# Performance work log

Hardware: AMD Instinct MI355X
Metric: run time of the kernel (lower is better)

Reference implementation:

```python
import jax, jax.numpy as jnp
import numpy as np

B, T, IN_DIM, D, C = 64, 128, 300, 64, 10
NUM_LAYERS = 2   # recurrent_cells = [QRNNCell(d)] * num_layers -> SHARED cell params
BETA = 0.8       # QActivation beta; scale_factor=2 -> matrix square of rho


def _ortho(k, n, m):
    a = jax.random.normal(k, (n, n), dtype=jnp.float32)
    q, _ = jnp.linalg.qr(a)
    return q[:, :m]


def setup_inputs() -> dict:
    key = jax.random.key(0)
    ks = jax.random.split(key, 8)
    return {
        "x": jax.random.normal(ks[0], (B, T, IN_DIM), jnp.float32),
        "amp_w": jax.random.normal(ks[1], (IN_DIM, D), jnp.float32) * (1.0 / np.sqrt(IN_DIM)),
        "amp_b": jnp.zeros((D,), jnp.float32),
        "phase_w": jax.random.normal(ks[2], (IN_DIM, D), jnp.float32) * (1.0 / np.sqrt(IN_DIM)),
        "phase_b": jnp.zeros((D,), jnp.float32),
        "unitary_x": _ortho(ks[3], D, D),   # real orthogonal (Stiefel) unitary
        "unitary_h": _ortho(ks[4], D, D),
        "cell_lambda": jnp.zeros((), jnp.float32),
        "dense_w": _ortho(ks[5], D, C),     # orthonormal columns: D -> C subspace map
        "dense_lambda": jnp.zeros((), jnp.float32),
        "meas_kernel": jax.random.normal(ks[6], (C, C, 2), jnp.float32),  # complex measurement vectors
    }


def _uconj(U, r, i):
    # real unitary conjugation U rho U^T applied to complex rho = r + 1j*i
    return (jnp.einsum('pq,bqr,sr->bps', U, r, U),
            jnp.einsum('pq,bqr,sr->bps', U, i, U))


def _qactivation(r, i):
    # scale_factor=2: rho^2 (sharpens eigen-spectrum), trace-normalized; beta-mix with rho
    r2 = r @ r - i @ i
    i2 = r @ i + i @ r
    tr = jnp.trace(r2, axis1=-2, axis2=-1)[..., None, None]
    return BETA * r2 / tr + (1.0 - BETA) * r, BETA * i2 / tr + (1.0 - BETA) * i


def _run_layer(xs_r, xs_i, Ux, Uh, lam):
    # xs_*: [T,B,D,D]; sequential QRNN scan over time
    b, d = xs_r.shape[1], xs_r.shape[-1]
    h0 = (jnp.broadcast_to(jnp.eye(d, dtype=xs_r.dtype) / d, (b, d, d)),
          jnp.zeros((b, d, d), xs_r.dtype))
    def step(h, x):
        xr, xi = x
        hr, hi = h
        uxr, uxi = _uconj(Ux, xr, xi)
        uhr, uhi = _uconj(Uh, hr, hi)
        nr = lam * uxr + (1.0 - lam) * uhr
        ni = lam * uxi + (1.0 - lam) * uhi
        nr, ni = _qactivation(nr, ni)
        return (nr, ni), (nr, ni)
    _, (out_r, out_i) = jax.lax.scan(step, h0, (xs_r, xs_i))
    return out_r, out_i


def reference(x, amp_w, amp_b, phase_w, phase_b, unitary_x, unitary_h,
              cell_lambda, dense_w, dense_lambda, meas_kernel):
    # amplitude (L2-normalized) and phase projections
    amp = x @ amp_w + amp_b
    amp = amp / jnp.linalg.norm(amp, axis=-1, keepdims=True)
    phase = x @ phase_w + phase_b
    sr = amp * jnp.cos(phase)                      # ComplexMultiply -> [B,T,D]
    si = amp * jnp.sin(phase)
    # QOuter: pure density matrices rho = |s><s| -> [T,B,D,D]
    rr = jnp.einsum('btd,bte->tbde', sr, sr) + jnp.einsum('btd,bte->tbde', si, si)
    ri = jnp.einsum('btd,bte->tbde', si, sr) - jnp.einsum('btd,bte->tbde', sr, si)
    lam = jax.nn.sigmoid(cell_lambda)
    for _ in range(NUM_LAYERS):                    # shared cell params (list * num_layers)
        rr, ri = _run_layer(rr, ri, unitary_x, unitary_h, lam)
    # QDropout: identity in eval mode
    # QDense: sigma = W^T rho W, Lambda-mixed with I/C, trace-normalized
    c = dense_w.shape[1]
    sg_r = jnp.einsum('dc,tbde,ef->tbcf', dense_w, rr, dense_w)
    sg_i = jnp.einsum('dc,tbde,ef->tbcf', dense_w, ri, dense_w)
    dlam = jax.nn.sigmoid(dense_lambda)
    sg_r = dlam * sg_r + (1.0 - dlam) * jnp.eye(c, dtype=sg_r.dtype) / c
    sg_i = dlam * sg_i
    tr = jnp.trace(sg_r, axis1=-2, axis2=-1)[..., None, None]
    sg_r = sg_r / tr
    sg_i = sg_i / tr
    # QMeasurement: p_k = Re(<v_k| rho |v_k>) with unit-norm complex v_k
    vr, vi = meas_kernel[..., 0], meas_kernel[..., 1]
    nrm = jnp.sqrt(jnp.sum(vr * vr + vi * vi, axis=-1, keepdims=True))
    vr, vi = vr / nrm, vi / nrm
    p = (jnp.einsum('kc,kd,tbcd->tbk', vr, vr, sg_r)
         + jnp.einsum('kc,kd,tbcd->tbk', vi, vi, sg_r)
         - jnp.einsum('kc,kd,tbcd->tbk', vr, vi, sg_i)
         + jnp.einsum('kc,kd,tbcd->tbk', vi, vr, sg_i))
    return jnp.log(jnp.transpose(p, (1, 0, 2)))    # [B,T,C] log-probs
```

## Files before the change

kernel.cpp:

```cpp
#include <hip/hip_runtime.h>
#include <math.h>

#define B_ 64
#define T_ 128
#define INDIM 300
#define D_ 64
#define C_ 10
#define BETA_ 0.8f

typedef unsigned int u32;
typedef _Float16 half8 __attribute__((ext_vector_type(8)));
typedef float f32x4 __attribute__((ext_vector_type(4)));
typedef u32 u32x4 __attribute__((ext_vector_type(4)));
typedef u32 u32x2 __attribute__((ext_vector_type(2)));

#define GIDX(cb,kc,ln) ((((cb)*2+(kc))*64) + (ln))

struct Frag { half8 h, l; };

static __device__ __forceinline__ float sigmoidf_(float x){ return 1.f/(1.f+expf(-x)); }

static __device__ __forceinline__ float wave_sum(float v){
#pragma unroll
  for (int off = 32; off > 0; off >>= 1) v += __shfl_down(v, off);
  return v;
}

static __device__ __forceinline__ u32 pkh(_Float16 a, _Float16 b){
  unsigned short ba = __builtin_bit_cast(unsigned short, a);
  unsigned short bb = __builtin_bit_cast(unsigned short, b);
  return (u32)ba | ((u32)bb << 16);
}

static __device__ __forceinline__ void split4(const float* x, u32x2& hw, u32x2& lw){
  _Float16 h0=(_Float16)x[0], h1=(_Float16)x[1], h2=(_Float16)x[2], h3=(_Float16)x[3];
  _Float16 l0=(_Float16)(x[0]-(float)h0), l1=(_Float16)(x[1]-(float)h1);
  _Float16 l2=(_Float16)(x[2]-(float)h2), l3=(_Float16)(x[3]-(float)h3);
  hw[0]=pkh(h0,h1); hw[1]=pkh(h2,h3); lw[0]=pkh(l0,l1); lw[1]=pkh(l2,l3);
}

static __device__ __forceinline__ void up2v(u32 hw, u32 lw, float& v0, float& v1){
  _Float16 h0=__builtin_bit_cast(_Float16,(unsigned short)(hw & 0xffffu));
  _Float16 h1=__builtin_bit_cast(_Float16,(unsigned short)(hw >> 16));
  _Float16 l0=__builtin_bit_cast(_Float16,(unsigned short)(lw & 0xffffu));
  _Float16 l1=__builtin_bit_cast(_Float16,(unsigned short)(lw >> 16));
  v0 = (float)h0 + (float)l0;
  v1 = (float)h1 + (float)l1;
}

static __device__ __forceinline__ void mfma4(const Frag& a, const Frag& b, f32x4& acc){
  acc = __builtin_amdgcn_mfma_f32_16x16x32_f16(a.h, b.h, acc, 0, 0, 0);
  acc = __builtin_amdgcn_mfma_f32_16x16x32_f16(a.h, b.l, acc, 0, 0, 0);
  acc = __builtin_amdgcn_mfma_f32_16x16x32_f16(a.l, b.h, acc, 0, 0, 0);
}

static __device__ __forceinline__ Frag ldfrag(const u32* buf, int g, bool neg){
  u32x4 a = *reinterpret_cast<const u32x4*>(buf + g*4);
  u32x4 b = *reinterpret_cast<const u32x4*>(buf + 2048 + g*4);
  if (neg){
#pragma unroll
    for (int i=0;i<4;++i){ a[i]^=0x80008000u; b[i]^=0x80008000u; }
  }
  Frag f; f.h = __builtin_bit_cast(half8, a); f.l = __builtin_bit_cast(half8, b);
  return f;
}

static __device__ __forceinline__ Frag ldbg(const u32* FL, int grp, int lane){
  const u32* p = FL + ((size_t)(grp*64 + lane))*8;
  u32x4 a = *reinterpret_cast<const u32x4*>(p);
  u32x4 b = *reinterpret_cast<const u32x4*>(p+4);
  Frag f; f.h = __builtin_bit_cast(half8, a); f.l = __builtin_bit_cast(half8, b);
  return f;
}

static __device__ __forceinline__ void store_tile(u32* O, int ti, int tj, int h, int c15,
                                                  const float* x){
  const int s = h & 1;
  const int lp = c15 + 16*((2*ti + (h>>1)) & 3);
  const int g = GIDX(tj, ti>>1, lp);
  u32x2 hw, lw; split4(x, hw, lw);
  *reinterpret_cast<u32x2*>(O + g*4 + 2*s) = hw;
  *reinterpret_cast<u32x2*>(O + 2048 + g*4 + 2*s) = lw;
}

static __device__ __forceinline__ void read_tile(const u32* O, int ti, int tj, int h, int c15,
                                                 float* n){
  const int s = h & 1;
  const int lp = c15 + 16*((2*ti + (h>>1)) & 3);
  const int g = GIDX(tj, ti>>1, lp);
  u32x2 nh = *reinterpret_cast<const u32x2*>(O + g*4 + 2*s);
  u32x2 nl = *reinterpret_cast<const u32x2*>(O + 2048 + g*4 + 2*s);
  up2v(nh[0],nl[0],n[0],n[1]); up2v(nh[1],nl[1],n[2],n[3]);
}

__global__ __launch_bounds__(64) void proj_kernel(
    const float* __restrict__ x, const float* __restrict__ amp_w,
    const float* __restrict__ amp_b, const float* __restrict__ phase_w,
    const float* __restrict__ phase_b, const float* __restrict__ Ux,
    float* __restrict__ u_out) {
    __shared__ float xr[INDIM];
    __shared__ float s_r[D_], s_i[D_];
    const int bt = blockIdx.x;
    const int b = bt / T_, t = bt % T_;
    const float* xrow = x + (size_t)bt * INDIM;
    for (int i = threadIdx.x; i < INDIM; i += 64) xr[i] = xrow[i];
    __syncthreads();
    const int d = threadIdx.x;
    float a = amp_b[d], p = phase_b[d];
    for (int k = 0; k < INDIM; ++k) {
        float xv = xr[k];
        a = fmaf(xv, amp_w[k * D_ + d], a);
        p = fmaf(xv, phase_w[k * D_ + d], p);
    }
    float sq = a * a;
    #pragma unroll
    for (int off = 32; off > 0; off >>= 1) sq += __shfl_xor(sq, off);
    float an = a / sqrtf(sq);
    s_r[d] = an * cosf(p);
    s_i[d] = an * sinf(p);
    __syncthreads();
    float ur = 0.f, ui = 0.f;
    const float* Uxrow = Ux + d * D_;
    for (int e = 0; e < D_; ++e) {
        float uv = Uxrow[e];
        ur = fmaf(uv, s_r[e], ur);
        ui = fmaf(uv, s_i[e], ui);
    }
    float* ub = u_out + ((size_t)t * B_ + b) * 128;
    ub[d] = ur;
    ub[64 + d] = ui;
}

__global__ __launch_bounds__(256) void setup_kernel(
    const float* __restrict__ Uh, const float* __restrict__ Ux,
    const float* __restrict__ W, const float* __restrict__ meas,
    u32* __restrict__ UhFL, u32* __restrict__ UxFL,
    u32* __restrict__ AB2FL, float* __restrict__ AB2p, float* __restrict__ ABt)
{
  const int tid = threadIdx.x;
  for (int wi = tid; wi < 4096; wi += 256){
    int off = wi & 7, g = wi >> 3;
    int lane_ = g & 63, cbkc = g >> 6;
    int cb = cbkc >> 1, kc = cbkc & 1;
    int wq = off & 3; bool isHi = off < 4;
    int k0 = 32*kc + 8*(lane_>>4) + 2*wq;
    int c  = 16*cb + (lane_&15);
    {
      float x0 = Uh[c*64 + k0], x1 = Uh[c*64 + k0 + 1];
      _Float16 h0=(_Float16)x0, h1=(_Float16)x1;
      UhFL[wi] = isHi ? pkh(h0,h1)
                      : pkh((_Float16)(x0-(float)h0), (_Float16)(x1-(float)h1));
    }
    {
      float x0 = Ux[c*64 + k0], x1 = Ux[c*64 + k0 + 1];
      _Float16 h0=(_Float16)x0, h1=(_Float16)x1;
      UxFL[wi] = isHi ? pkh(h0,h1)
                      : pkh((_Float16)(x0-(float)h0), (_Float16)(x1-(float)h1));
    }
  }
  __shared__ float invn[C_];
  if (tid < C_) {
    float s = 0.f;
    for (int j = 0; j < C_; ++j) {
      float vr = meas[(tid * C_ + j) * 2], vi = meas[(tid * C_ + j) * 2 + 1];
      s += vr * vr + vi * vi;
    }
    invn[tid] = 1.0f / sqrtf(s);
  }
  __syncthreads();
  for (int i = tid; i < D_ * 32; i += 256) {
    int dd = i >> 5, c = i & 31;
    float v = 0.f;
    if (c < C_) {
      float acc = 0.f;
      for (int j = 0; j < C_; ++j) acc = fmaf(W[dd * C_ + j], meas[(c * C_ + j) * 2], acc);
      v = acc * invn[c];
    } else if (c < 2 * C_) {
      int k = c - C_;
      float acc = 0.f;
      for (int j = 0; j < C_; ++j) acc = fmaf(W[dd * C_ + j], meas[(k * C_ + j) * 2 + 1], acc);
      v = acc * invn[k];
    } else if (c < 3 * C_) {
      v = W[dd * C_ + (c - 2 * C_)];
    }
    AB2p[i] = v;
  }
  __syncthreads();
  for (int wi = tid; wi < 2048; wi += 256){
    int off = wi & 7, g = wi >> 3;
    int lane_ = g & 63, cbkc = g >> 6;
    int cb = cbkc >> 1, kc = cbkc & 1;
    int wq = off & 3; bool isHi = off < 4;
    int k0 = 32*kc + 8*(lane_>>4) + 2*wq;
    int c  = 16*cb + (lane_&15);
    float x0 = AB2p[k0*32 + c], x1 = AB2p[(k0+1)*32 + c];
    _Float16 h0=(_Float16)x0, h1=(_Float16)x1;
    AB2FL[wi] = isHi ? pkh(h0,h1)
                     : pkh((_Float16)(x0-(float)h0), (_Float16)(x1-(float)h1));
  }
  for (int i = tid; i < 30*64; i += 256){
    int c = i >> 6, d = i & 63;
    ABt[i] = AB2p[d*32 + c];
  }
}

__global__ __launch_bounds__(512) void qrnn_kernel(
    const float* __restrict__ u_in,
    const u32* __restrict__ UhFL, const u32* __restrict__ UxFL,
    const u32* __restrict__ AB2FL, const float* __restrict__ ABt,
    const float* __restrict__ cell_lambda, const float* __restrict__ dense_lambda,
    float* __restrict__ out)
{
  __shared__ __align__(16) u32 ds[9*4096];
  __shared__ float u_lds[128];
  __shared__ float scrN1[8], scrNp[8], scrQ[12];

  const int tid = threadIdx.x;
  const int lane = tid & 63;
  const int w = tid >> 6;
  const int h = lane >> 4;
  const int c15 = lane & 15;
  const int bidx = blockIdx.x;
  const float lam = sigmoidf_(cell_lambda[0]);
  const float clm = 1.f - lam;
  const float dlam = sigmoidf_(dense_lambda[0]);

  u32* const B0 = ds + 0*4096;
  u32* const B1 = ds + 1*4096;
  u32* const B2 = ds + 2*4096;
  u32* const B3 = ds + 3*4096;
  u32* const B4 = ds + 4*4096;
  u32* const B5 = ds + 5*4096;
  u32* const B6 = ds + 6*4096;
  u32* const B7 = ds + 7*4096;
  u32* const B8 = ds + 8*4096;
  float* const Zt = reinterpret_cast<float*>(B6);

  const u32 one64 = (u32)__builtin_bit_cast(unsigned short, (_Float16)0.015625f);
  for (int wi = tid; wi < 4096; wi += 512){
    u32 vR = 0u;
    if (wi < 2048){
      int g = wi >> 2, wq = wi & 3;
      int lane_ = g & 63, cbkc = g >> 6;
      int cb = cbkc >> 1, kc = cbkc & 1;
      int k0 = 32*kc + 8*(lane_>>4) + 2*wq;
      int c = 16*cb + (lane_&15);
      if (k0 == c)   vR |= one64;
      if (k0+1 == c) vR |= (one64 << 16);
    }
    B0[wi] = vR; B2[wi] = vR; B1[wi] = 0u; B3[wi] = 0u;
  }
  __syncthreads();

  for (int t = 0; t <= T_; ++t){
    const bool doMain = (t < T_);
    const bool doTail = (t > 0);
    const int par = t & 1;
    u32* const pH2I = par ? B4 : B3;
    u32* const pTXR = par ? B3 : B4;

    if (doMain){
      if (tid < 128) u_lds[tid] = u_in[((size_t)t*B_ + bidx)*128 + tid];
      const int comp = w>>2, ti = w&3;
      const u32* A = comp ? B1 : B0;
      Frag a0 = ldfrag(A, GIDX(ti,0,lane), false);
      Frag a1 = ldfrag(A, GIDX(ti,1,lane), false);
      u32* O = comp ? B5 : pTXR;
#pragma unroll
      for (int tj=0;tj<4;++tj){
        Frag b0 = ldbg(UhFL, tj*2+0, lane);
        Frag b1 = ldbg(UhFL, tj*2+1, lane);
        f32x4 acc = {0.f,0.f,0.f,0.f};
        mfma4(a0,b0,acc); mfma4(a1,b1,acc);
        float xv[4] = {acc[0],acc[1],acc[2],acc[3]};
        store_tile(O, ti, tj, h, c15, xv);
      }
    }
    if (doTail){
      const int rb = w;
      const int cb = rb&3;
      const u32* A = (rb<4) ? B2 : pH2I;
      Frag a0 = ldfrag(A, GIDX(cb,0,lane), false);
      Frag a1 = ldfrag(A, GIDX(cb,1,lane), false);
#pragma unroll
      for (int cz=0;cz<2;++cz){
        Frag b0 = ldbg(AB2FL, cz*2+0, lane);
        Frag b1 = ldbg(AB2FL, cz*2+1, lane);
        f32x4 za = {0.f,0.f,0.f,0.f};
        mfma4(a0,b0,za); mfma4(a1,b1,za);
        const int c = 16*cz + c15;
        if (c < 30){
          float* zp = Zt + c*129 + 16*rb + 4*h;
#pragma unroll
          for (int rr=0;rr<4;++rr) zp[rr] = za[rr];
        }
      }
    }
    __syncthreads();

    if (doMain){
      const int comp = w>>2, ti = w&3;
      const u32* A = comp ? B5 : pTXR;
      Frag a0 = ldfrag(A, GIDX(ti,0,lane), false);
      Frag a1 = ldfrag(A, GIDX(ti,1,lane), false);
      u32* O = comp ? B8 : B7;
      float uR[4], uI[4];
#pragma unroll
      for (int rr=0;rr<4;++rr){
        uR[rr] = u_lds[16*ti + 4*h + rr];
        uI[rr] = u_lds[64 + 16*ti + 4*h + rr];
      }
      float ss = 0.f;
#pragma unroll
      for (int tj=0;tj<4;++tj){
        Frag b0 = ldbg(UhFL, tj*2+0, lane);
        Frag b1 = ldbg(UhFL, tj*2+1, lane);
        f32x4 acc = {0.f,0.f,0.f,0.f};
        mfma4(a0,b0,acc); mfma4(a1,b1,acc);
        const float urc = u_lds[16*tj + c15], uic = u_lds[64 + 16*tj + c15];
        float xv[4];
#pragma unroll
        for (int rr=0;rr<4;++rr){
          float ov = comp ? (uI[rr]*urc - uR[rr]*uic) : (uR[rr]*urc + uI[rr]*uic);
          xv[rr] = lam*ov + clm*acc[rr];
          ss = fmaf(xv[rr], xv[rr], ss);
        }
        store_tile(O, ti, tj, h, c15, xv);
      }
      ss = wave_sum(ss);
      if (lane == 0) scrN1[w] = ss;
    }
    if (doTail){
      {
        const int k = w;
        float av = ABt[k*64 + lane], bv = ABt[(10+k)*64 + lane];
        float v = av*Zt[k*129 + lane] + bv*Zt[(10+k)*129 + lane]
                + av*Zt[(10+k)*129 + 64 + lane] - bv*Zt[k*129 + 64 + lane];
        v = wave_sum(v);
        if (lane == 0) scrQ[k] = v;
      }
      if (w < 2){
        const int k = 8 + w;
        float av = ABt[k*64 + lane], bv = ABt[(10+k)*64 + lane];
        float v = av*Zt[k*129 + lane] + bv*Zt[(10+k)*129 + lane]
                + av*Zt[(10+k)*129 + 64 + lane] - bv*Zt[k*129 + 64 + lane];
        v = wave_sum(v);
        if (lane == 0) scrQ[k] = v;
      } else if (w == 2){
        float v = 0.f;
#pragma unroll
        for (int cc=0; cc<10; ++cc)
          v = fmaf(ABt[(20+cc)*64 + lane], Zt[(20+cc)*129 + lane], v);
        v = wave_sum(v);
        if (lane == 0) scrQ[10] = v;
      }
    }
    __syncthreads();

    if (doMain){
      const int o = w>>2, tj = w&3;
      f32x4 acc[4];
#pragma unroll
      for (int i=0;i<4;++i) acc[i] = f32x4{0.f,0.f,0.f,0.f};
#pragma unroll
      for (int m=0;m<2;++m){
        const u32* Ab = m ? B8 : B7;
        const u32* Bb = o ? (m ? B7 : B8) : (m ? B8 : B7);
        const bool neg = (o==1) && (m==1);
#pragma unroll
        for (int kc=0;kc<2;++kc){
          Frag bf = ldfrag(Bb, GIDX(tj,kc,lane), false);
#pragma unroll
          for (int i=0;i<4;++i){
            Frag af = ldfrag(Ab, GIDX(i,kc,lane), neg);
            mfma4(af, bf, acc[i]);
          }
        }
      }
      const f32x4* sv = reinterpret_cast<const f32x4*>(scrN1);
      f32x4 s4 = sv[0] + sv[1];
      const float trv = s4[0]+s4[1]+s4[2]+s4[3];
      const float sb = BETA_/trv, cbm = 1.f - BETA_;
      const u32* Nsrc = o ? B8 : B7;
      u32* Od = o ? B1 : B0;
#pragma unroll
      for (int i=0;i<4;++i){
        float n[4]; read_tile(Nsrc, i, tj, h, c15, n);
        float xv[4];
#pragma unroll
        for (int rr=0;rr<4;++rr) xv[rr] = fmaf(sb, acc[i][rr], cbm*n[rr]);
        store_tile(Od, i, tj, h, c15, xv);
      }
    }
    if (doTail && tid < 10){
      float pnum = dlam*scrQ[tid] + (1.f-dlam)*0.1f;
      float pden = dlam*scrQ[10] + (1.f-dlam);
      out[((size_t)bidx*T_ + (t-1))*C_ + tid] = logf(pnum/pden);
    }
    __syncthreads();

    if (doMain){
      {
        const int g2 = w>>2, comp=(w>>1)&1, th=w&1;
        const u32* A = g2 ? (comp? pH2I : B2) : (comp? B1 : B0);
        const u32* FL = g2 ? UhFL : UxFL;
        u32* O = g2 ? (comp? B7 : B6) : (comp? B5 : pTXR);
        Frag a00 = ldfrag(A, GIDX(th,0,lane),   false);
        Frag a01 = ldfrag(A, GIDX(th,1,lane),   false);
        Frag a10 = ldfrag(A, GIDX(th+2,0,lane), false);
        Frag a11 = ldfrag(A, GIDX(th+2,1,lane), false);
#pragma unroll
        for (int tj=0;tj<4;++tj){
          Frag b0 = ldbg(FL, tj*2+0, lane);
          Frag b1 = ldbg(FL, tj*2+1, lane);
          f32x4 acc0 = {0.f,0.f,0.f,0.f};
          mfma4(a00,b0,acc0); mfma4(a01,b1,acc0);
          float xv0[4] = {acc0[0],acc0[1],acc0[2],acc0[3]};
          store_tile(O, th, tj, h, c15, xv0);
          f32x4 acc1 = {0.f,0.f,0.f,0.f};
          mfma4(a10,b0,acc1); mfma4(a11,b1,acc1);
          float xv1[4] = {acc1[0],acc1[1],acc1[2],acc1[3]};
          store_tile(O, th+2, tj, h, c15, xv1);
        }
      }
      __syncthreads();

      {
        const int comp = w>>2, ti = w&3;
        u32* O = comp ? pH2I : B8;
        const u32* AX = comp ? B5 : pTXR;
        const u32* AH = comp ? B7 : B6;
        Frag ax0 = ldfrag(AX, GIDX(ti,0,lane), false);
        Frag ax1 = ldfrag(AX, GIDX(ti,1,lane), false);
        Frag ah0 = ldfrag(AH, GIDX(ti,0,lane), false);
        Frag ah1 = ldfrag(AH, GIDX(ti,1,lane), false);
        float ss = 0.f;
#pragma unroll
        for (int tj=0;tj<4;++tj){
          f32x4 aX = {0.f,0.f,0.f,0.f};
          {
            Frag bx0 = ldbg(UxFL, tj*2+0, lane);
            Frag bx1 = ldbg(UxFL, tj*2+1, lane);
            mfma4(ax0,bx0,aX); mfma4(ax1,bx1,aX);
          }
          f32x4 aH = {0.f,0.f,0.f,0.f};
          {
            Frag bh0 = ldbg(UhFL, tj*2+0, lane);
            Frag bh1 = ldbg(UhFL, tj*2+1, lane);
            mfma4(ah0,bh0,aH); mfma4(ah1,bh1,aH);
          }
          float xv[4];
#pragma unroll
          for (int rr=0;rr<4;++rr){
            xv[rr] = lam*aX[rr] + clm*aH[rr];
            ss = fmaf(xv[rr], xv[rr], ss);
          }
          store_tile(O, ti, tj, h, c15, xv);
        }
        ss = wave_sum(ss);
        if (lane == 0) scrNp[w] = ss;
      }
      __syncthreads();

      {
        const int o = w>>2, tj = w&3;
        const u32* NPR = B8;
        const u32* NPI = pH2I;
        f32x4 acc[4];
#pragma unroll
        for (int i=0;i<4;++i) acc[i] = f32x4{0.f,0.f,0.f,0.f};
#pragma unroll
        for (int m=0;m<2;++m){
          const u32* Ab = m ? NPI : NPR;
          const u32* Bb = o ? (m ? NPR : NPI) : (m ? NPI : NPR);
          const bool neg = (o==1) && (m==1);
#pragma unroll
          for (int kc=0;kc<2;++kc){
            Frag bf = ldfrag(Bb, GIDX(tj,kc,lane), false);
#pragma unroll
            for (int i=0;i<4;++i){
              Frag af = ldfrag(Ab, GIDX(i,kc,lane), neg);
              mfma4(af, bf, acc[i]);
            }
          }
        }
        const f32x4* sv = reinterpret_cast<const f32x4*>(scrNp);
        f32x4 s4 = sv[0] + sv[1];
        const float trv = s4[0]+s4[1]+s4[2]+s4[3];
        const float sb = BETA_/trv, cbm = 1.f - BETA_;
        const u32* Nsrc = o ? NPI : NPR;
        u32* Od = o ? pTXR : B2;
#pragma unroll
        for (int i=0;i<4;++i){
          float n[4]; read_tile(Nsrc, i, tj, h, c15, n);
          float xv[4];
#pragma unroll
          for (int rr=0;rr<4;++rr) xv[rr] = fmaf(sb, acc[i][rr], cbm*n[rr]);
          store_tile(Od, i, tj, h, c15, xv);
        }
      }
      __syncthreads();
    }
  }
}

extern "C" void kernel_launch(void* const* d_in, const int* in_sizes, int n_in,
                              void* d_out, int out_size, void* d_ws, size_t ws_size,
                              hipStream_t stream) {
    const float* x       = (const float*)d_in[0];
    const float* amp_w   = (const float*)d_in[1];
    const float* amp_b   = (const float*)d_in[2];
    const float* phase_w = (const float*)d_in[3];
    const float* phase_b = (const float*)d_in[4];
    const float* Ux      = (const float*)d_in[5];
    const float* Uh      = (const float*)d_in[6];
    const float* cl      = (const float*)d_in[7];
    const float* W       = (const float*)d_in[8];
    const float* dl      = (const float*)d_in[9];
    const float* meas    = (const float*)d_in[10];

    float* ws   = (float*)d_ws;
    float* u    = ws;
    u32*  UhFL  = (u32*)(ws + 1048576);
    u32*  UxFL  = UhFL + 4096;
    u32*  AB2FL = UxFL + 4096;
    float* AB2p = (float*)(AB2FL + 2048);
    float* ABt  = AB2p + 2048;
    float* out  = (float*)d_out;

    proj_kernel<<<B_ * T_, 64, 0, stream>>>(x, amp_w, amp_b, phase_w, phase_b, Ux, u);
    setup_kernel<<<1, 256, 0, stream>>>(Uh, Ux, W, meas, UhFL, UxFL, AB2FL, AB2p, ABt);
    qrnn_kernel<<<B_, 512, 0, stream>>>(u, UhFL, UxFL, AB2FL, ABt, cl, dl, out);
}
```

Before: 1.662 ms.

## Use 2x2 output tiles per wave and cache unitary high halves in registers

Each wave now computes a 2x2 block of 16x16 output tiles instead of a full row or column strip. This cuts the A- and B-fragment loads per MFMA in every matmul stage of the recurrent step. The high-precision halves of the Uh and Ux fragments are preloaded once into registers for the whole time loop, so only the low halves are reloaded from global memory. The split-f16 MFMA order changes slightly and register pressure rises, which could lower occupancy or cause spills.

```diff
diff --git a/kernel.cpp b/kernel.cpp
--- a/kernel.cpp
+++ b/kernel.cpp
@@ -54,6 +54,12 @@
   acc = __builtin_amdgcn_mfma_f32_16x16x32_f16(a.l, b.h, acc, 0, 0, 0);
 }
 
+static __device__ __forceinline__ void mfma3(const Frag& a, half8 bh, half8 bl, f32x4& acc){
+  acc = __builtin_amdgcn_mfma_f32_16x16x32_f16(a.h, bh, acc, 0, 0, 0);
+  acc = __builtin_amdgcn_mfma_f32_16x16x32_f16(a.l, bh, acc, 0, 0, 0);
+  acc = __builtin_amdgcn_mfma_f32_16x16x32_f16(a.h, bl, acc, 0, 0, 0);
+}
+
 static __device__ __forceinline__ Frag ldfrag(const u32* buf, int g, bool neg){
   u32x4 a = *reinterpret_cast<const u32x4*>(buf + g*4);
   u32x4 b = *reinterpret_cast<const u32x4*>(buf + 2048 + g*4);
@@ -71,6 +77,16 @@
   u32x4 b = *reinterpret_cast<const u32x4*>(p+4);
   Frag f; f.h = __builtin_bit_cast(half8, a); f.l = __builtin_bit_cast(half8, b);
   return f;
+}
+
+static __device__ __forceinline__ half8 ldbg_hi(const u32* FL, int grp, int lane){
+  u32x4 a = *reinterpret_cast<const u32x4*>(FL + ((size_t)(grp*64 + lane))*8);
+  return __builtin_bit_cast(half8, a);
+}
+
+static __device__ __forceinline__ half8 ldbg_lo(const u32* FL, int grp, int lane){
+  u32x4 b = *reinterpret_cast<const u32x4*>(FL + ((size_t)(grp*64 + lane))*8 + 4);
+  return __builtin_bit_cast(half8, b);
 }
 
 static __device__ __forceinline__ void store_tile(u32* O, int ti, int tj, int h, int c15,
@@ -225,6 +241,12 @@
   const float clm = 1.f - lam;
   const float dlam = sigmoidf_(dense_lambda[0]);
 
+  const int comp = w >> 2;
+  const int q = w & 3;
+  const int hi2 = q >> 1;
+  const int hj2 = q & 1;
+  const int ti0 = 2*hi2, tj0 = 2*hj2;
+
   u32* const B0 = ds + 0*4096;
   u32* const B1 = ds + 1*4096;
   u32* const B2 = ds + 2*4096;
@@ -235,6 +257,15 @@
   u32* const B7 = ds + 7*4096;
   u32* const B8 = ds + 8*4096;
   float* const Zt = reinterpret_cast<float*>(B6);
+
+  half8 UhPh[2][2], UxPh[2][2];
+#pragma unroll
+  for (int tjj=0;tjj<2;++tjj)
+#pragma unroll
+    for (int kc=0;kc<2;++kc){
+      UhPh[tjj][kc] = ldbg_hi(UhFL, (tj0+tjj)*2+kc, lane);
+      UxPh[tjj][kc] = ldbg_hi(UxFL, (tj0+tjj)*2+kc, lane);
+    }
 
   const u32 one64 = (u32)__builtin_bit_cast(unsigned short, (_Float16)0.015625f);
   for (int wi = tid; wi < 4096; wi += 512){
@@ -261,20 +292,31 @@
 
     if (doMain){
       if (tid < 128) u_lds[tid] = u_in[((size_t)t*B_ + bidx)*128 + tid];
-      const int comp = w>>2, ti = w&3;
       const u32* A = comp ? B1 : B0;
-      Frag a0 = ldfrag(A, GIDX(ti,0,lane), false);
-      Frag a1 = ldfrag(A, GIDX(ti,1,lane), false);
       u32* O = comp ? B5 : pTXR;
-#pragma unroll
-      for (int tj=0;tj<4;++tj){
-        Frag b0 = ldbg(UhFL, tj*2+0, lane);
-        Frag b1 = ldbg(UhFL, tj*2+1, lane);
-        f32x4 acc = {0.f,0.f,0.f,0.f};
-        mfma4(a0,b0,acc); mfma4(a1,b1,acc);
-        float xv[4] = {acc[0],acc[1],acc[2],acc[3]};
-        store_tile(O, ti, tj, h, c15, xv);
-      }
+      f32x4 acc[2][2];
+#pragma unroll
+      for (int i=0;i<2;++i)
+#pragma unroll
+        for (int j=0;j<2;++j) acc[i][j] = f32x4{0.f,0.f,0.f,0.f};
+#pragma unroll
+      for (int kc=0;kc<2;++kc){
+        Frag a0 = ldfrag(A, GIDX(ti0,  kc, lane), false);
+        Frag a1 = ldfrag(A, GIDX(ti0+1,kc, lane), false);
+#pragma unroll
+        for (int tjj=0;tjj<2;++tjj){
+          half8 bl = ldbg_lo(UhFL, (tj0+tjj)*2+kc, lane);
+          mfma3(a0, UhPh[tjj][kc], bl, acc[0][tjj]);
+          mfma3(a1, UhPh[tjj][kc], bl, acc[1][tjj]);
+        }
+      }
+#pragma unroll
+      for (int i=0;i<2;++i)
+#pragma unroll
+        for (int j=0;j<2;++j){
+          float xv[4] = {acc[i][j][0],acc[i][j][1],acc[i][j][2],acc[i][j][3]};
+          store_tile(O, ti0+i, tj0+j, h, c15, xv);
+        }
     }
     if (doTail){
       const int rb = w;
@@ -299,33 +341,47 @@
     __syncthreads();
 
     if (doMain){
-      const int comp = w>>2, ti = w&3;
       const u32* A = comp ? B5 : pTXR;
-      Frag a0 = ldfrag(A, GIDX(ti,0,lane), false);
-      Frag a1 = ldfrag(A, GIDX(ti,1,lane), false);
       u32* O = comp ? B8 : B7;
-      float uR[4], uI[4];
-#pragma unroll
-      for (int rr=0;rr<4;++rr){
-        uR[rr] = u_lds[16*ti + 4*h + rr];
-        uI[rr] = u_lds[64 + 16*ti + 4*h + rr];
+      f32x4 acc[2][2];
+#pragma unroll
+      for (int i=0;i<2;++i)
+#pragma unroll
+        for (int j=0;j<2;++j) acc[i][j] = f32x4{0.f,0.f,0.f,0.f};
+#pragma unroll
+      for (int kc=0;kc<2;++kc){
+        Frag a0 = ldfrag(A, GIDX(ti0,  kc, lane), false);
+        Frag a1 = ldfrag(A, GIDX(ti0+1,kc, lane), false);
+#pragma unroll
+        for (int tjj=0;tjj<2;++tjj){
+          half8 bl = ldbg_lo(UhFL, (tj0+tjj)*2+kc, lane);
+          mfma3(a0, UhPh[tjj][kc], bl, acc[0][tjj]);
+          mfma3(a1, UhPh[tjj][kc], bl, acc[1][tjj]);
+        }
       }
       float ss = 0.f;
 #pragma unroll
-      for (int tj=0;tj<4;++tj){
-        Frag b0 = ldbg(UhFL, tj*2+0, lane);
-        Frag b1 = ldbg(UhFL, tj*2+1, lane);
-        f32x4 acc = {0.f,0.f,0.f,0.f};
-        mfma4(a0,b0,acc); mfma4(a1,b1,acc);
-        const float urc = u_lds[16*tj + c15], uic = u_lds[64 + 16*tj + c15];
-        float xv[4];
+      for (int i=0;i<2;++i){
+        const int ti = ti0+i;
+        float uR[4], uI[4];
 #pragma unroll
         for (int rr=0;rr<4;++rr){
-          float ov = comp ? (uI[rr]*urc - uR[rr]*uic) : (uR[rr]*urc + uI[rr]*uic);
-          xv[rr] = lam*ov + clm*acc[rr];
-          ss = fmaf(xv[rr], xv[rr], ss);
-        }
-        store_tile(O, ti, tj, h, c15, xv);
+          uR[rr] = u_lds[16*ti + 4*h + rr];
+          uI[rr] = u_lds[64 + 16*ti + 4*h + rr];
+        }
+#pragma unroll
+        for (int j=0;j<2;++j){
+          const int tj = tj0+j;
+          const float urc = u_lds[16*tj + c15], uic = u_lds[64 + 16*tj + c15];
+          float xv[4];
+#pragma unroll
+          for (int rr=0;rr<4;++rr){
+            float ov = comp ? (uI[rr]*urc - uR[rr]*uic) : (uR[rr]*urc + uI[rr]*uic);
+            xv[rr] = lam*ov + clm*acc[i][j][rr];
+            ss = fmaf(xv[rr], xv[rr], ss);
+          }
+          store_tile(O, ti, tj, h, c15, xv);
+        }
       }
       ss = wave_sum(ss);
       if (lane == 0) scrN1[w] = ss;
@@ -358,10 +414,12 @@
     __syncthreads();
 
     if (doMain){
-      const int o = w>>2, tj = w&3;
-      f32x4 acc[4];
-#pragma unroll
-      for (int i=0;i<4;++i) acc[i] = f32x4{0.f,0.f,0.f,0.f};
+      const int o = comp;
+      f32x4 acc[2][2];
+#pragma unroll
+      for (int i=0;i<2;++i)
+#pragma unroll
+        for (int j=0;j<2;++j) acc[i][j] = f32x4{0.f,0.f,0.f,0.f};
 #pragma unroll
       for (int m=0;m<2;++m){
         const u32* Ab = m ? B8 : B7;
@@ -369,12 +427,12 @@
         const bool neg = (o==1) && (m==1);
 #pragma unroll
         for (int kc=0;kc<2;++kc){
-          Frag bf = ldfrag(Bb, GIDX(tj,kc,lane), false);
-#pragma unroll
-          for (int i=0;i<4;++i){
-            Frag af = ldfrag(Ab, GIDX(i,kc,lane), neg);
-            mfma4(af, bf, acc[i]);
-          }
+          Frag a0 = ldfrag(Ab, GIDX(ti0,  kc, lane), neg);
+          Frag a1 = ldfrag(Ab, GIDX(ti0+1,kc, lane), neg);
+          Frag b0 = ldfrag(Bb, GIDX(tj0,  kc, lane), false);
+          Frag b1 = ldfrag(Bb, GIDX(tj0+1,kc, lane), false);
+          mfma4(a0,b0,acc[0][0]); mfma4(a0,b1,acc[0][1]);
+          mfma4(a1,b0,acc[1][0]); mfma4(a1,b1,acc[1][1]);
         }
       }
       const f32x4* sv = reinterpret_cast<const f32x4*>(scrN1);
@@ -384,13 +442,15 @@
       const u32* Nsrc = o ? B8 : B7;
       u32* Od = o ? B1 : B0;
 #pragma unroll
-      for (int i=0;i<4;++i){
-        float n[4]; read_tile(Nsrc, i, tj, h, c15, n);
-        float xv[4];
-#pragma unroll
-        for (int rr=0;rr<4;++rr) xv[rr] = fmaf(sb, acc[i][rr], cbm*n[rr]);
-        store_tile(Od, i, tj, h, c15, xv);
-      }
+      for (int i=0;i<2;++i)
+#pragma unroll
+        for (int j=0;j<2;++j){
+          float n[4]; read_tile(Nsrc, ti0+i, tj0+j, h, c15, n);
+          float xv[4];
+#pragma unroll
+          for (int rr=0;rr<4;++rr) xv[rr] = fmaf(sb, acc[i][j][rr], cbm*n[rr]);
+          store_tile(Od, ti0+i, tj0+j, h, c15, xv);
+        }
     }
     if (doTail && tid < 10){
       float pnum = dlam*scrQ[tid] + (1.f-dlam)*0.1f;
@@ -401,74 +461,117 @@
 
     if (doMain){
       {
-        const int g2 = w>>2, comp=(w>>1)&1, th=w&1;
-        const u32* A = g2 ? (comp? pH2I : B2) : (comp? B1 : B0);
-        const u32* FL = g2 ? UhFL : UxFL;
-        u32* O = g2 ? (comp? B7 : B6) : (comp? B5 : pTXR);
-        Frag a00 = ldfrag(A, GIDX(th,0,lane),   false);
-        Frag a01 = ldfrag(A, GIDX(th,1,lane),   false);
-        Frag a10 = ldfrag(A, GIDX(th+2,0,lane), false);
-        Frag a11 = ldfrag(A, GIDX(th+2,1,lane), false);
-#pragma unroll
-        for (int tj=0;tj<4;++tj){
-          Frag b0 = ldbg(FL, tj*2+0, lane);
-          Frag b1 = ldbg(FL, tj*2+1, lane);
-          f32x4 acc0 = {0.f,0.f,0.f,0.f};
-          mfma4(a00,b0,acc0); mfma4(a01,b1,acc0);
-          float xv0[4] = {acc0[0],acc0[1],acc0[2],acc0[3]};
-          store_tile(O, th, tj, h, c15, xv0);
-          f32x4 acc1 = {0.f,0.f,0.f,0.f};
-          mfma4(a10,b0,acc1); mfma4(a11,b1,acc1);
-          float xv1[4] = {acc1[0],acc1[1],acc1[2],acc1[3]};
-          store_tile(O, th+2, tj, h, c15, xv1);
-        }
+        f32x4 acc[2][2];
+        const u32* A1 = comp ? B1 : B0;
+        u32* O1 = comp ? B5 : pTXR;
+#pragma unroll
+        for (int i=0;i<2;++i)
+#pragma unroll
+          for (int j=0;j<2;++j) acc[i][j] = f32x4{0.f,0.f,0.f,0.f};
+#pragma unroll
+        for (int kc=0;kc<2;++kc){
+          Frag a0 = ldfrag(A1, GIDX(ti0,  kc, lane), false);
+          Frag a1 = ldfrag(A1, GIDX(ti0+1,kc, lane), false);
+#pragma unroll
+          for (int tjj=0;tjj<2;++tjj){
+            half8 bl = ldbg_lo(UxFL, (tj0+tjj)*2+kc, lane);
+            mfma3(a0, UxPh[tjj][kc], bl, acc[0][tjj]);
+            mfma3(a1, UxPh[tjj][kc], bl, acc[1][tjj]);
+          }
+        }
+#pragma unroll
+        for (int i=0;i<2;++i)
+#pragma unroll
+          for (int j=0;j<2;++j){
+            float xv[4] = {acc[i][j][0],acc[i][j][1],acc[i][j][2],acc[i][j][3]};
+            store_tile(O1, ti0+i, tj0+j, h, c15, xv);
+          }
+        const u32* A2 = comp ? pH2I : B2;
+        u32* O2 = comp ? B7 : B6;
+#pragma unroll
+        for (int i=0;i<2;++i)
+#pragma unroll
+          for (int j=0;j<2;++j) acc[i][j] = f32x4{0.f,0.f,0.f,0.f};
+#pragma unroll
+        for (int kc=0;kc<2;++kc){
+          Frag a0 = ldfrag(A2, GIDX(ti0,  kc, lane), false);
+          Frag a1 = ldfrag(A2, GIDX(ti0+1,kc, lane), false);
+#pragma unroll
+          for (int tjj=0;tjj<2;++tjj){
+            half8 bl = ldbg_lo(UhFL, (tj0+tjj)*2+kc, lane);
+            mfma3(a0, UhPh[tjj][kc], bl, acc[0][tjj]);
+            mfma3(a1, UhPh[tjj][kc], bl, acc[1][tjj]);
+          }
+        }
+#pragma unroll
+        for (int i=0;i<2;++i)
+#pragma unroll
+          for (int j=0;j<2;++j){
+            float xv[4] = {acc[i][j][0],acc[i][j][1],acc[i][j][2],acc[i][j][3]};
+            store_tile(O2, ti0+i, tj0+j, h, c15, xv);
+          }
       }
       __syncthreads();
 
       {
-        const int comp = w>>2, ti = w&3;
         u32* O = comp ? pH2I : B8;
         const u32* AX = comp ? B5 : pTXR;
         const u32* AH = comp ? B7 : B6;
-        Frag ax0 = ldfrag(AX, GIDX(ti,0,lane), false);
-        Frag ax1 = ldfrag(AX, GIDX(ti,1,lane), false);
-        Frag ah0 = ldfrag(AH, GIDX(ti,0,lane), false);
-        Frag ah1 = ldfrag(AH, GIDX(ti,1,lane), false);
+        f32x4 aXc[2][2], aHc[2][2];
+#pragma unroll
+        for (int i=0;i<2;++i)
+#pragma unroll
+          for (int j=0;j<2;++j){ aXc[i][j]=f32x4{0.f,0.f,0.f,0.f}; aHc[i][j]=f32x4{0.f,0.f,0.f,0.f}; }
+#pragma unroll
+        for (int kc=0;kc<2;++kc){
+          {
+            Frag x0 = ldfrag(AX, GIDX(ti0,  kc, lane), false);
+            Frag x1 = ldfrag(AX, GIDX(ti0+1,kc, lane), false);
+#pragma unroll
+            for (int tjj=0;tjj<2;++tjj){
+              half8 bl = ldbg_lo(UxFL, (tj0+tjj)*2+kc, lane);
+              mfma3(x0, UxPh[tjj][kc], bl, aXc[0][tjj]);
+              mfma3(x1, UxPh[tjj][kc], bl, aXc[1][tjj]);
+            }
+          }
+          {
+            Frag h0f = ldfrag(AH, GIDX(ti0,  kc, lane), false);
+            Frag h1f = ldfrag(AH, GIDX(ti0+1,kc, lane), false);
+#pragma unroll
+            for (int tjj=0;tjj<2;++tjj){
+              half8 bl = ldbg_lo(UhFL, (tj0+tjj)*2+kc, lane);
+              mfma3(h0f, UhPh[tjj][kc], bl, aHc[0][tjj]);
+              mfma3(h1f, UhPh[tjj][kc], bl, aHc[1][tjj]);
+            }
+          }
+        }
         float ss = 0.f;
 #pragma unroll
-        for (int tj=0;tj<4;++tj){
-          f32x4 aX = {0.f,0.f,0.f,0.f};
-          {
-            Frag bx0 = ldbg(UxFL, tj*2+0, lane);
-            Frag bx1 = ldbg(UxFL, tj*2+1, lane);
-            mfma4(ax0,bx0,aX); mfma4(ax1,bx1,aX);
-          }
-          f32x4 aH = {0.f,0.f,0.f,0.f};
-          {
-            Frag bh0 = ldbg(UhFL, tj*2+0, lane);
-            Frag bh1 = ldbg(UhFL, tj*2+1, lane);
-            mfma4(ah0,bh0,aH); mfma4(ah1,bh1,aH);
-          }
-          float xv[4];
-#pragma unroll
-          for (int rr=0;rr<4;++rr){
-            xv[rr] = lam*aX[rr] + clm*aH[rr];
-            ss = fmaf(xv[rr], xv[rr], ss);
-          }
-          store_tile(O, ti, tj, h, c15, xv);
-        }
+        for (int i=0;i<2;++i)
+#pragma unroll
+          for (int j=0;j<2;++j){
+            float xv[4];
+#pragma unroll
+            for (int rr=0;rr<4;++rr){
+              xv[rr] = lam*aXc[i][j][rr] + clm*aHc[i][j][rr];
+              ss = fmaf(xv[rr], xv[rr], ss);
+            }
+            store_tile(O, ti0+i, tj0+j, h, c15, xv);
+          }
         ss = wave_sum(ss);
         if (lane == 0) scrNp[w] = ss;
       }
       __syncthreads();
 
       {
-        const int o = w>>2, tj = w&3;
+        const int o = comp;
         const u32* NPR = B8;
         const u32* NPI = pH2I;
-        f32x4 acc[4];
-#pragma unroll
-        for (int i=0;i<4;++i) acc[i] = f32x4{0.f,0.f,0.f,0.f};
+        f32x4 acc[2][2];
+#pragma unroll
+        for (int i=0;i<2;++i)
+#pragma unroll
+          for (int j=0;j<2;++j) acc[i][j] = f32x4{0.f,0.f,0.f,0.f};
 #pragma unroll
         for (int m=0;m<2;++m){
           const u32* Ab = m ? NPI : NPR;
@@ -476,12 +579,12 @@
           const bool neg = (o==1) && (m==1);
 #pragma unroll
           for (int kc=0;kc<2;++kc){
-            Frag bf = ldfrag(Bb, GIDX(tj,kc,lane), false);
-#pragma unroll
-            for (int i=0;i<4;++i){
-              Frag af = ldfrag(Ab, GIDX(i,kc,lane), neg);
-              mfma4(af, bf, acc[i]);
-            }
+            Frag a0 = ldfrag(Ab, GIDX(ti0,  kc, lane), neg);
+            Frag a1 = ldfrag(Ab, GIDX(ti0+1,kc, lane), neg);
+            Frag b0 = ldfrag(Bb, GIDX(tj0,  kc, lane), false);
+            Frag b1 = ldfrag(Bb, GIDX(tj0+1,kc, lane), false);
+            mfma4(a0,b0,acc[0][0]); mfma4(a0,b1,acc[0][1]);
+            mfma4(a1,b0,acc[1][0]); mfma4(a1,b1,acc[1][1]);
           }
         }
         const f32x4* sv = reinterpret_cast<const f32x4*>(scrNp);
@@ -491,13 +594,15 @@
         const u32* Nsrc = o ? NPI : NPR;
         u32* Od = o ? pTXR : B2;
 #pragma unroll
-        for (int i=0;i<4;++i){
-          float n[4]; read_tile(Nsrc, i, tj, h, c15, n);
-          float xv[4];
-#pragma unroll
-          for (int rr=0;rr<4;++rr) xv[rr] = fmaf(sb, acc[i][rr], cbm*n[rr]);
-          store_tile(Od, i, tj, h, c15, xv);
-        }
+        for (int i=0;i<2;++i)
+#pragma unroll
+          for (int j=0;j<2;++j){
+            float n[4]; read_tile(Nsrc, ti0+i, tj0+j, h, c15, n);
+            float xv[4];
+#pragma unroll
+            for (int rr=0;rr<4;++rr) xv[rr] = fmaf(sb, acc[i][j][rr], cbm*n[rr]);
+            store_tile(Od, ti0+i, tj0+j, h, c15, xv);
+          }
       }
       __syncthreads();
     }
```

After: 1.340 ms. 1.24x faster.
